# Performance work log

Hardware: AMD Instinct MI355X
Metric: run time of the kernel (lower is better)

## Reference

```python
import jax, jax.numpy as jnp
import numpy as np

B, S, H, STEPS = 4096, 169, 64, 24  # batch, input seq (window 168 + covariate row), hidden, rollout steps


def _lstm(xseq, Wih, Whh, bih, bhh, h0, c0):
    """PyTorch-style single-layer LSTM. xseq: [B,T,D] -> ([B,T,H], hT, cT). Gate order i,f,g,o."""
    xg = jnp.einsum('btd,gd->btg', xseq, Wih) + (bih + bhh)  # precompute input proj [B,T,4H]

    def step(carry, xg_t):
        h, c = carry
        g = xg_t + h @ Whh.T
        i, f, gg, o = jnp.split(g, 4, axis=-1)
        c = jax.nn.sigmoid(f) * c + jax.nn.sigmoid(i) * jnp.tanh(gg)
        h = jax.nn.sigmoid(o) * jnp.tanh(c)
        return (h, c), h

    (hT, cT), hs = jax.lax.scan(step, (h0, c0), jnp.swapaxes(xg, 0, 1))
    return jnp.swapaxes(hs, 0, 1), hT, cT


def reference(x, Wih1, Whh1, bih1, bhh1, Wih2, Whh2, bih2, bhh2, fc1_w, fc1_b, fc2_w, fc2_b):
    win, d = x[:, :-1, :], x[:, -1, :]  # [B,168,1], [B,1]
    z = jnp.zeros((x.shape[0], H), x.dtype)

    def outer(win, _):
        h1s, h1, c1 = _lstm(win, Wih1, Whh1, bih1, bhh1, z, z)
        h1s = jax.nn.relu(h1s)
        # lstm2 is seeded with lstm1's final (h, c) state, as in the torch code
        h2s, _, _ = _lstm(h1s, Wih2, Whh2, bih2, bhh2, h1, c1)
        feat = jnp.concatenate([jax.nn.relu(h2s[:, -1, :]), d], axis=1)  # [B,65]
        out = (feat @ fc1_w.T + fc1_b) @ fc2_w.T + fc2_b  # [B,1] (no relu between fc1/fc2)
        win = jnp.concatenate([win[:, 1:, :], out[:, :, None]], axis=1)  # slide window
        return win, out[:, 0]

    _, outs = jax.lax.scan(outer, win, None, length=STEPS)  # outs: [24,B]
    return jnp.swapaxes(outs, 0, 1)  # [B,24]


def setup_inputs() -> dict:
    key = jax.random.key(0)
    ks = jax.random.split(key, 14)
    bnd = 1.0 / np.sqrt(H)

    def u(k, shape):
        return jax.random.uniform(k, shape, jnp.float32, -bnd, bnd)

    return {
        'x': jax.random.normal(ks[0], (B, S, 1), jnp.float32),
        'Wih1': u(ks[1], (4 * H, 1)),
        'Whh1': u(ks[2], (4 * H, H)),
        'bih1': u(ks[3], (4 * H,)),
        'bhh1': u(ks[4], (4 * H,)),
        'Wih2': u(ks[5], (4 * H, H)),
        'Whh2': u(ks[6], (4 * H, H)),
        'bih2': u(ks[7], (4 * H,)),
        'bhh2': u(ks[8], (4 * H,)),
        'fc1_w': u(ks[9], (64, 65)),
        'fc1_b': u(ks[10], (64,)),
        'fc2_w': u(ks[11], (1, 64)),
        'fc2_b': u(ks[12], (1,)),
    }
```

## Files before the change

### kernel.cpp

```cpp
#include <hip/hip_runtime.h>
#include <stdint.h>

#define NB 16
#define WIN 168
#define NSTEPS 24
#define NBLK (4096/NB)
#define NT 512

typedef __attribute__((ext_vector_type(8))) short bf16x8;
typedef __attribute__((ext_vector_type(4))) float f32x4;

#if __has_builtin(__builtin_amdgcn_rcpf)
#define RCPF(x) __builtin_amdgcn_rcpf(x)
#else
#define RCPF(x) (1.0f / (x))
#endif
#if __has_builtin(__builtin_amdgcn_exp2f)
#define EXP2F(x) __builtin_amdgcn_exp2f(x)
#else
#define EXP2F(x) __expf((x) * 0.6931471805599453f)
#endif

__device__ __forceinline__ float sigm(float x){
  return RCPF(1.0f + EXP2F(x * -1.4426950408889634f));
}
__device__ __forceinline__ float sigtanh(float a, float b){
  float A = EXP2F(a * -1.4426950408889634f);
  float B = EXP2F(fabsf(b) * -2.8853900817779268f);
  float t = (1.0f - B) * RCPF((1.0f + A) * (1.0f + B));
  return __builtin_copysignf(t, b);
}

__device__ __forceinline__ uint32_t bf_rn(float f){
  uint32_t u = __builtin_bit_cast(uint32_t, f);
  return (u + 0x7FFFu + ((u >> 16) & 1u)) >> 16;
}
__device__ __forceinline__ float bf_f(uint32_t s){
  return __builtin_bit_cast(float, s << 16);
}
__device__ __forceinline__ void split_t(float f, uint32_t& hi, uint32_t& lo){
  uint32_t u = __builtin_bit_cast(uint32_t, f);
  hi = u >> 16;
  lo = bf_rn(f - bf_f(hi));
}
__device__ __forceinline__ void split_s(float f, short& hi, short& lo){
  uint32_t h = bf_rn(f);
  hi = (short)h;
  lo = (short)bf_rn(f - bf_f(h));
}
__device__ __forceinline__ uint32_t cvtpk2(float a, float b){
  uint32_t r;
  asm("v_cvt_pk_bf16_f32 %0, %1, %2" : "=v"(r) : "v"(a), "v"(b));
  return r;
}
__device__ __forceinline__ float hi_even(uint32_t p){
  return __builtin_bit_cast(float, p << 16);
}
__device__ __forceinline__ float hi_odd(uint32_t p){
  return __builtin_bit_cast(float, p & 0xFFFF0000u);
}
__device__ __forceinline__ f32x4 mfma16(bf16x8 a, bf16x8 b, f32x4 c){
  return __builtin_amdgcn_mfma_f32_16x16x32_bf16(a, b, c, 0, 0, 0);
}

__device__ __forceinline__ void lstm_epi(const f32x4 acc[4], float c[4], float hn[4]){
  #pragma unroll
  for (int r = 0; r < 4; r++){
    float cn = __builtin_fmaf(sigm(acc[1][r]), c[r], sigtanh(acc[0][r], acc[2][r]));
    c[r] = cn;
    hn[r] = sigtanh(acc[3][r], cn);
  }
}

#define FROW 136
#define FBLK 544
#define FB(buf,hl,kt) ((((buf)*2 + (hl))*2 + (kt)) * FBLK)
#define BUF_INTS (2*FBLK)

__global__ __launch_bounds__(NT, 2) void lstm_fused_kernel(
  const float* __restrict__ x,    const float* __restrict__ Wih1, const float* __restrict__ Whh1,
  const float* __restrict__ bih1, const float* __restrict__ bhh1,
  const float* __restrict__ Wih2, const float* __restrict__ Whh2,
  const float* __restrict__ bih2, const float* __restrict__ bhh2,
  const float* __restrict__ fc1w, const float* __restrict__ fc1b,
  const float* __restrict__ fc2w, const float* __restrict__ fc2b,
  float* __restrict__ out, short* __restrict__ hist)
{
  __shared__ __align__(16) short aS[2*2*2*FBLK];
  __shared__ __align__(16) short bS[2*2*2*FBLK];
  __shared__ float cS[64][16];
  __shared__ float win_s[WIN][NB];
  __shared__ float Hlast[NB][68];
  __shared__ float fc1w_s[64*68];
  __shared__ float dval_s[NB];

  const int tid = threadIdx.x;
  const int wv8 = tid >> 6;
  const int wv  = wv8 & 3;
  const bool isA = (wv8 < 4);
  const int ln  = tid & 63;
  const int q   = ln >> 4;
  const int n   = ln & 15;
  const int bg0 = blockIdx.x * NB;
  const int u0  = 16*wv + 4*q;
  const int kt_  = u0 >> 5;
  const int q2_  = (u0 >> 3) & 3;
  const int jj0_ = u0 & 7;
  const int rdo  = q*FROW + n*8;
  const int wro  = q2_*FROW + n*8 + jj0_;
  const int gwo  = kt_*512 + q2_*128 + n*8 + jj0_;
  const int ro   = q*128 + n*8;
  short* __restrict__ hblk = hist + (size_t)blockIdx.x * WIN * 2048;

  for (int i = tid; i < WIN*NB; i += NT){ int t = i >> 4, b = i & 15; win_s[t][b] = x[(bg0 + b)*169 + t]; }
  for (int i = tid; i < 64*65; i += NT){ int j = i / 65, k = i % 65; fc1w_s[j*68 + k] = fc1w[i]; }
  if (tid < NB) dval_s[tid] = x[(bg0 + tid)*169 + 168];

  const float fc1b_r = fc1b[ln];
  const float fc2w_r = fc2w[ln];
  const float fc2b_r = fc2b[0];

  auto fc_head = [&](int s){
    float o2[2];
    #pragma unroll
    for (int bi = 0; bi < 2; bi++){
      const int b = 2*wv8 + bi;
      float a1 = fc1b_r;
      #pragma unroll
      for (int k4 = 0; k4 < 16; k4++){
        const float* wp = &fc1w_s[ln*68 + k4*4];
        const float* hp = &Hlast[b][k4*4];
        a1 += wp[0]*hp[0] + wp[1]*hp[1] + wp[2]*hp[2] + wp[3]*hp[3];
      }
      a1 += dval_s[b] * fc1w_s[ln*68 + 64];
      float v = a1 * fc2w_r;
      #pragma unroll
      for (int off = 32; off > 0; off >>= 1) v += __shfl_xor(v, off);
      o2[bi] = v + fc2b_r;
    }
    if (ln == 0){
      #pragma unroll
      for (int bi = 0; bi < 2; bi++){
        const int b = 2*wv8 + bi;
        out[(bg0 + b)*24 + s] = o2[bi];
        win_s[s % WIN][b] = o2[bi];
      }
    }
  };

  if (isA){
    bf16x8 A1hi[4][2], A1lo[4][2], Ain1[4];
    f32x4 b1c[4];
    #pragma unroll
    for (int e = 0; e < 4; e++){
      const int ja = 64*e + 16*wv + n;
      #pragma unroll
      for (int kt = 0; kt < 2; kt++){
        const float* pw = Whh1 + ja*64 + kt*32 + q*8;
        #pragma unroll
        for (int jj = 0; jj < 8; jj++){ short h,l; split_s(pw[jj], h, l); A1hi[e][kt][jj] = h; A1lo[e][kt][jj] = l; }
      }
      bf16x8 ain = {0,0,0,0,0,0,0,0};
      if (q == 0){ short wh, wl; split_s(Wih1[ja], wh, wl); ain[0] = wh; ain[1] = wh; ain[2] = wl; }
      Ain1[e] = ain;
      const int jc = 64*e + u0;
      #pragma unroll
      for (int r = 0; r < 4; r++) b1c[e][r] = bih1[jc+r] + bhh1[jc+r];
    }
    float c1[4];

    auto lstm1 = [&](int rb, int wb, int slot, int t, bool first){
      f32x4 acc[4];
      bf16x8 bin = {0,0,0,0,0,0,0,0};
      { float xv = win_s[slot][n];
        uint32_t xp = cvtpk2(xv, xv);
        float rx = xv - hi_even(xp);
        uint32_t xq = cvtpk2(rx, rx);
        if (q == 0){ bin[0] = (short)xp; bin[1] = (short)xq; bin[2] = (short)xp; } }
      if (first){
        #pragma unroll
        for (int e = 0; e < 4; e++) acc[e] = mfma16(Ain1[e], bin, b1c[e]);
      } else {
        bf16x8 Bh0 = *(const bf16x8*)&aS[FB(rb,0,0)+rdo];
        bf16x8 Bl0 = *(const bf16x8*)&aS[FB(rb,1,0)+rdo];
        bf16x8 Bh1 = *(const bf16x8*)&aS[FB(rb,0,1)+rdo];
        bf16x8 Bl1 = *(const bf16x8*)&aS[FB(rb,1,1)+rdo];
        #pragma unroll
        for (int e = 0; e < 4; e++){
          f32x4 a = b1c[e];
          a = mfma16(A1hi[e][0], Bh0, a);
          a = mfma16(A1hi[e][0], Bl0, a);
          a = mfma16(A1lo[e][0], Bh0, a);
          a = mfma16(A1hi[e][1], Bh1, a);
          a = mfma16(A1hi[e][1], Bl1, a);
          a = mfma16(A1lo[e][1], Bh1, a);
          a = mfma16(Ain1[e], bin, a);
          acc[e] = a;
        }
      }
      float hn[4];
      lstm_epi(acc, c1, hn);
      uint32_t p01 = cvtpk2(hn[0], hn[1]);
      uint32_t p23 = cvtpk2(hn[2], hn[3]);
      float r0 = hn[0] - hi_even(p01), r1 = hn[1] - hi_odd(p01);
      float r2 = hn[2] - hi_even(p23), r3 = hn[3] - hi_odd(p23);
      uint32_t q01 = cvtpk2(r0, r1);
      uint32_t q23 = cvtpk2(r2, r3);
      *(uint2*)&aS[FB(wb,0,kt_)+wro] = make_uint2(p01, p23);
      *(uint2*)&aS[FB(wb,1,kt_)+wro] = make_uint2(q01, q23);
      uint32_t m01 = (hn[0] > 0.0f ? 0x0000FFFFu : 0u) | (hn[1] > 0.0f ? 0xFFFF0000u : 0u);
      uint32_t m23 = (hn[2] > 0.0f ? 0x0000FFFFu : 0u) | (hn[3] > 0.0f ? 0xFFFF0000u : 0u);
      short* Hp = hblk + (size_t)t * 2048;
      *(uint2*)&Hp[gwo]        = make_uint2(p01 & m01, p23 & m23);
      *(uint2*)&Hp[1024 + gwo] = make_uint2(q01 & m01, q23 & m23);
    };

    #pragma unroll
    for (int r = 0; r < 4; r++) c1[r] = 0.0f;
    __syncthreads();
    lstm1(0, 1, 0, 0, true);
    for (int t = 1; t < WIN-1; t += 2){
      __syncthreads();
      lstm1(1, 0, t, t, false);
      __syncthreads();
      lstm1(0, 1, t+1, t+1, false);
    }
    __syncthreads();
    lstm1(1, 0, WIN-1, WIN-1, false);
    #pragma unroll
    for (int r = 0; r < 4; r++) cS[u0 + r][n] = c1[r];

    for (int sg = 1; sg < NSTEPS; sg++){
      #pragma unroll
      for (int r = 0; r < 4; r++) c1[r] = 0.0f;
      int slot = sg;
      __syncthreads();
      lstm1(0, 1, slot, 0, true);
      slot++;
      for (int t = 1; t < WIN-1; t += 2){
        __syncthreads();
        lstm1(1, 0, slot, t, false);
        slot++; if (slot == WIN) slot = 0;
        __syncthreads();
        lstm1(0, 1, slot, t+1, false);
        slot++; if (slot == WIN) slot = 0;
      }
      __syncthreads();
      __syncthreads();
      fc_head(sg - 1);
      __syncthreads();
      lstm1(1, 0, slot, WIN-1, false);
      #pragma unroll
      for (int r = 0; r < 4; r++) cS[u0 + r][n] = c1[r];
    }

    for (int i = 0; i < WIN + 1; i++) __syncthreads();
    fc_head(NSTEPS - 1);

  } else {
    bf16x8 A2hi[4][4], A2lo[4][4];
    f32x4 b2c[4];
    #pragma unroll
    for (int e = 0; e < 4; e++){
      const int ja = 64*e + 16*wv + n;
      #pragma unroll
      for (int kt = 0; kt < 4; kt++){
        const float* pw = (kt < 2 ? (Wih2 + ja*64 + kt*32) : (Whh2 + ja*64 + (kt-2)*32)) + q*8;
        #pragma unroll
        for (int jj = 0; jj < 8; jj++){ short h,l; split_s(pw[jj], h, l); A2hi[e][kt][jj] = h; A2lo[e][kt][jj] = l; }
      }
      const int jc = 64*e + u0;
      #pragma unroll
      for (int r = 0; r < 4; r++) b2c[e][r] = bih2[jc+r] + bhh2[jc+r];
    }
    float c2[4];
    bf16x8 ch0, cl0, ch1, cl1, nh0, nl0, nh1, nl1;

    auto loadc = [&](int t){
      const short* Hp = hblk + (size_t)t * 2048;
      ch0 = *(const bf16x8*)&Hp[ro];
      cl0 = *(const bf16x8*)&Hp[1024 + ro];
      ch1 = *(const bf16x8*)&Hp[512 + ro];
      cl1 = *(const bf16x8*)&Hp[1536 + ro];
    };
    auto loadn = [&](int t){
      const short* Hp = hblk + (size_t)t * 2048;
      nh0 = *(const bf16x8*)&Hp[ro];
      nl0 = *(const bf16x8*)&Hp[1024 + ro];
      nh1 = *(const bf16x8*)&Hp[512 + ro];
      nl1 = *(const bf16x8*)&Hp[1536 + ro];
    };
    auto shift = [&](){ ch0 = nh0; cl0 = nl0; ch1 = nh1; cl1 = nl1; };

    auto lstm2 = [&](const short* Sr, int rb, short* Sw, int wb, bool last){
      bf16x8 L2h0 = *(const bf16x8*)&Sr[FB(rb,0,0)+rdo];
      bf16x8 L2l0 = *(const bf16x8*)&Sr[FB(rb,1,0)+rdo];
      bf16x8 L2h1 = *(const bf16x8*)&Sr[FB(rb,0,1)+rdo];
      bf16x8 L2l1 = *(const bf16x8*)&Sr[FB(rb,1,1)+rdo];
      f32x4 acc[4];
      #pragma unroll
      for (int e = 0; e < 4; e++){
        f32x4 a = b2c[e];
        a = mfma16(A2hi[e][0], ch0, a);
        a = mfma16(A2hi[e][0], cl0, a);
        a = mfma16(A2lo[e][0], ch0, a);
        a = mfma16(A2hi[e][1], ch1, a);
        a = mfma16(A2hi[e][1], cl1, a);
        a = mfma16(A2lo[e][1], ch1, a);
        a = mfma16(A2hi[e][2], L2h0, a);
        a = mfma16(A2hi[e][2], L2l0, a);
        a = mfma16(A2lo[e][2], L2h0, a);
        a = mfma16(A2hi[e][3], L2h1, a);
        a = mfma16(A2hi[e][3], L2l1, a);
        a = mfma16(A2lo[e][3], L2h1, a);
        acc[e] = a;
      }
      float hn[4];
      lstm_epi(acc, c2, hn);
      if (!last){
        uint32_t p01 = cvtpk2(hn[0], hn[1]);
        uint32_t p23 = cvtpk2(hn[2], hn[3]);
        float r0 = hn[0] - hi_even(p01), r1 = hn[1] - hi_odd(p01);
        float r2 = hn[2] - hi_even(p23), r3 = hn[3] - hi_odd(p23);
        *(uint2*)&Sw[FB(wb,0,kt_)+wro] = make_uint2(p01, p23);
        *(uint2*)&Sw[FB(wb,1,kt_)+wro] = make_uint2(cvtpk2(r0, r1), cvtpk2(r2, r3));
      } else {
        #pragma unroll
        for (int r = 0; r < 4; r++) Hlast[n][u0 + r] = fmaxf(hn[r], 0.0f);
      }
    };

    for (int i = 0; i < WIN; i++) __syncthreads();

    for (int sg = 1; sg < NSTEPS; sg++){
      loadc(0);
      loadn(1);
      __syncthreads();
      #pragma unroll
      for (int r = 0; r < 4; r++) c2[r] = cS[u0 + r][n];
      lstm2(aS, 0, bS, 1, false);
      shift();
      for (int t = 1; t < WIN-1; t += 2){
        __syncthreads();
        loadn(t + 1);
        lstm2(bS, 1, bS, 0, false);
        shift();
        __syncthreads();
        loadn(t + 2);
        lstm2(bS, 0, bS, 1, false);
        shift();
      }
      __syncthreads();
      lstm2(bS, 1, bS, 0, true);
      __syncthreads();
      fc_head(sg - 1);
      __syncthreads();
    }

    {
      loadc(0);
      loadn(1);
      __syncthreads();
      #pragma unroll
      for (int r = 0; r < 4; r++) c2[r] = cS[u0 + r][n];
      lstm2(aS, 0, bS, 1, false);
      shift();
      for (int t = 1; t < WIN-1; t += 2){
        __syncthreads();
        loadn(t + 1);
        lstm2(bS, 1, bS, 0, false);
        shift();
        __syncthreads();
        loadn(t + 2);
        lstm2(bS, 0, bS, 1, false);
        shift();
      }
      __syncthreads();
      lstm2(bS, 1, bS, 0, true);
      __syncthreads();
      fc_head(NSTEPS - 1);
    }
  }
}

__global__ __launch_bounds__(256, 1) void lstm_fallback_kernel(
  const float* __restrict__ x,    const float* __restrict__ Wih1, const float* __restrict__ Whh1,
  const float* __restrict__ bih1, const float* __restrict__ bhh1,
  const float* __restrict__ Wih2, const float* __restrict__ Whh2,
  const float* __restrict__ bih2, const float* __restrict__ bhh2,
  const float* __restrict__ fc1w, const float* __restrict__ fc1b,
  const float* __restrict__ fc2w, const float* __restrict__ fc2b,
  float* __restrict__ out)
{
  __shared__ __align__(16) short aS[2*2*2*FBLK];
  __shared__ __align__(16) short r1f[2*2*2*FBLK];
  __shared__ __align__(16) short rlf[2*2*2*FBLK];
  __shared__ float win_s[WIN][NB];
  __shared__ float Hlast[NB][68];
  __shared__ float fc1w_s[64*68];
  __shared__ float dval_s[NB];

  const int tid = threadIdx.x;
  const int wv  = tid >> 6;
  const int ln  = tid & 63;
  const int q   = ln >> 4;
  const int n   = ln & 15;
  const int bg0 = blockIdx.x * NB;
  const int u0  = 16*wv + 4*q;
  const int kt_  = u0 >> 5;
  const int q2_  = (u0 >> 3) & 3;
  const int jj0_ = u0 & 7;
  const int rdo  = q*FROW + n*8;
  const int wro  = q2_*FROW + n*8 + jj0_;

  for (int i = tid; i < WIN*NB; i += 256){ int t = i >> 4, b = i & 15; win_s[t][b] = x[(bg0 + b)*169 + t]; }
  for (int i = tid; i < 64*65; i += 256){ int j = i / 65, k = i % 65; fc1w_s[j*68 + k] = fc1w[i]; }
  if (tid < NB) dval_s[tid] = x[(bg0 + tid)*169 + 168];

  const float fc1b_r = fc1b[ln];
  const float fc2w_r = fc2w[ln];
  const float fc2b_r = fc2b[0];

  bf16x8 A1hi[4][2], A1lo[4][2], Ain1[4];
  bf16x8 A2hi[4][4], A2lo[4][4];
  f32x4 b1c[4], b2c[4];
  #pragma unroll
  for (int e = 0; e < 4; e++){
    const int ja = 64*e + 16*wv + n;
    #pragma unroll
    for (int kt = 0; kt < 2; kt++){
      const float* pw = Whh1 + ja*64 + kt*32 + q*8;
      #pragma unroll
      for (int jj = 0; jj < 8; jj++){ short h,l; split_s(pw[jj], h, l); A1hi[e][kt][jj] = h; A1lo[e][kt][jj] = l; }
    }
    #pragma unroll
    for (int kt = 0; kt < 4; kt++){
      const float* pw = (kt < 2 ? (Wih2 + ja*64 + kt*32) : (Whh2 + ja*64 + (kt-2)*32)) + q*8;
      #pragma unroll
      for (int jj = 0; jj < 8; jj++){ short h,l; split_s(pw[jj], h, l); A2hi[e][kt][jj] = h; A2lo[e][kt][jj] = l; }
    }
    bf16x8 ain = {0,0,0,0,0,0,0,0};
    if (q == 0){ short wh, wl; split_s(Wih1[ja], wh, wl); ain[0] = wh; ain[1] = wh; ain[2] = wl; }
    Ain1[e] = ain;
    const int jc = 64*e + u0;
    #pragma unroll
    for (int r = 0; r < 4; r++){
      b1c[e][r] = bih1[jc+r] + bhh1[jc+r];
      b2c[e][r] = bih2[jc+r] + bhh2[jc+r];
    }
  }

  float c1[4], c2[4], c1r[4];

  auto lstm1_step = [&](short* S, float* cst, int rb, int wb, int slot, bool relu_out){
    bf16x8 Bh0 = *(const bf16x8*)&S[FB(rb,0,0)+rdo];
    bf16x8 Bl0 = *(const bf16x8*)&S[FB(rb,1,0)+rdo];
    bf16x8 Bh1 = *(const bf16x8*)&S[FB(rb,0,1)+rdo];
    bf16x8 Bl1 = *(const bf16x8*)&S[FB(rb,1,1)+rdo];
    bf16x8 bin = {0,0,0,0,0,0,0,0};
    { float xv = win_s[slot][n]; uint32_t xh, xl; split_t(xv, xh, xl);
      if (q == 0){ bin[0] = (short)xh; bin[1] = (short)xl; bin[2] = (short)xh; } }
    f32x4 acc[4];
    #pragma unroll
    for (int e = 0; e < 4; e++){
      f32x4 a = b1c[e];
      a = mfma16(A1hi[e][0], Bh0, a);
      a = mfma16(A1hi[e][0], Bl0, a);
      a = mfma16(A1lo[e][0], Bh0, a);
      a = mfma16(A1hi[e][1], Bh1, a);
      a = mfma16(A1hi[e][1], Bl1, a);
      a = mfma16(A1lo[e][1], Bh1, a);
      a = mfma16(Ain1[e], bin, a);
      acc[e] = a;
    }
    float hn[4];
    lstm_epi(acc, cst, hn);
    uint32_t ph[4], pl[4];
    #pragma unroll
    for (int r = 0; r < 4; r++) split_t(hn[r], ph[r], pl[r]);
    *(uint2*)&S[FB(wb,0,kt_)+wro] = make_uint2(ph[0] | (ph[1]<<16), ph[2] | (ph[3]<<16));
    *(uint2*)&S[FB(wb,1,kt_)+wro] = make_uint2(pl[0] | (pl[1]<<16), pl[2] | (pl[3]<<16));
    if (relu_out){
      uint32_t sh[4], sl[4];
      #pragma unroll
      for (int r = 0; r < 4; r++){ bool pos = hn[r] > 0.0f; sh[r] = pos ? ph[r] : 0u; sl[r] = pos ? pl[r] : 0u; }
      *(uint2*)&rlf[FB(rb,0,kt_)+wro] = make_uint2(sh[0] | (sh[1]<<16), sh[2] | (sh[3]<<16));
      *(uint2*)&rlf[FB(rb,1,kt_)+wro] = make_uint2(sl[0] | (sl[1]<<16), sl[2] | (sl[3]<<16));
    }
  };

  auto lstm2_core = [&](bf16x8 L1h0, bf16x8 L1l0, bf16x8 L1h1, bf16x8 L1l1,
                        int rbuf, int wbuf, bool last){
    bf16x8 L2h0 = *(const bf16x8*)&aS[FB(rbuf,0,0)+rdo];
    bf16x8 L2l0 = *(const bf16x8*)&aS[FB(rbuf,1,0)+rdo];
    bf16x8 L2h1 = *(const bf16x8*)&aS[FB(rbuf,0,1)+rdo];
    bf16x8 L2l1 = *(const bf16x8*)&aS[FB(rbuf,1,1)+rdo];
    f32x4 acc[4];
    #pragma unroll
    for (int e = 0; e < 4; e++){
      f32x4 a = b2c[e];
      a = mfma16(A2hi[e][0], L1h0, a);
      a = mfma16(A2hi[e][0], L1l0, a);
      a = mfma16(A2lo[e][0], L1h0, a);
      a = mfma16(A2hi[e][1], L1h1, a);
      a = mfma16(A2hi[e][1], L1l1, a);
      a = mfma16(A2lo[e][1], L1h1, a);
      a = mfma16(A2hi[e][2], L2h0, a);
      a = mfma16(A2hi[e][2], L2l0, a);
      a = mfma16(A2lo[e][2], L2h0, a);
      a = mfma16(A2hi[e][3], L2h1, a);
      a = mfma16(A2hi[e][3], L2l1, a);
      a = mfma16(A2lo[e][3], L2h1, a);
      acc[e] = a;
    }
    float hn[4];
    lstm_epi(acc, c2, hn);
    if (!last){
      uint32_t ph[4], pl[4];
      #pragma unroll
      for (int r = 0; r < 4; r++) split_t(hn[r], ph[r], pl[r]);
      *(uint2*)&aS[FB(wbuf,0,kt_)+wro] = make_uint2(ph[0] | (ph[1]<<16), ph[2] | (ph[3]<<16));
      *(uint2*)&aS[FB(wbuf,1,kt_)+wro] = make_uint2(pl[0] | (pl[1]<<16), pl[2] | (pl[3]<<16));
    } else {
      #pragma unroll
      for (int r = 0; r < 4; r++) Hlast[n][u0 + r] = fmaxf(hn[r], 0.0f);
    }
  };

  for (int s = 0; s < NSTEPS; s++){
    { int* p = (int*)&aS[0];
      for (int i = tid; i < BUF_INTS; i += 256) p[i] = 0; }
    #pragma unroll
    for (int r = 0; r < 4; r++) c1[r] = 0.0f;
    int slot = s;
    for (int t = 0; t < WIN; t++){
      __syncthreads();
      lstm1_step(aS, c1, t & 1, (t & 1) ^ 1, slot, false);
      slot++; if (slot == WIN) slot = 0;
    }
    #pragma unroll
    for (int r = 0; r < 4; r++){ c2[r] = c1[r]; c1r[r] = 0.0f; }
    { int* p = (int*)&r1f[0];
      for (int i = tid; i < BUF_INTS; i += 256) p[i] = 0; }
    slot = s;
    __syncthreads();
    lstm1_step(r1f, c1r, 0, 1, slot, true);
    slot++;
    for (int i = 1; i < WIN; i++){
      __syncthreads();
      const int rb = i & 1, wb = rb ^ 1;
      lstm1_step(r1f, c1r, rb, wb, slot, true);
      bf16x8 L1h0 = *(const bf16x8*)&rlf[FB(wb,0,0)+rdo];
      bf16x8 L1l0 = *(const bf16x8*)&rlf[FB(wb,1,0)+rdo];
      bf16x8 L1h1 = *(const bf16x8*)&rlf[FB(wb,0,1)+rdo];
      bf16x8 L1l1 = *(const bf16x8*)&rlf[FB(wb,1,1)+rdo];
      lstm2_core(L1h0, L1l0, L1h1, L1l1, wb, rb, false);
      slot++; if (slot == WIN) slot = 0;
    }
    __syncthreads();
    {
      const int rb = (WIN - 1) & 1;
      bf16x8 L1h0 = *(const bf16x8*)&rlf[FB(rb,0,0)+rdo];
      bf16x8 L1l0 = *(const bf16x8*)&rlf[FB(rb,1,0)+rdo];
      bf16x8 L1h1 = *(const bf16x8*)&rlf[FB(rb,0,1)+rdo];
      bf16x8 L1l1 = *(const bf16x8*)&rlf[FB(rb,1,1)+rdo];
      lstm2_core(L1h0, L1l0, L1h1, L1l1, rb, 0, true);
    }
    __syncthreads();
    {
      float o4[4];
      #pragma unroll
      for (int bi = 0; bi < 4; bi++){
        const int b = 4*wv + bi;
        float a1 = fc1b_r;
        #pragma unroll
        for (int k4 = 0; k4 < 16; k4++){
          const float* wp = &fc1w_s[ln*68 + k4*4];
          const float* hp = &Hlast[b][k4*4];
          a1 += wp[0]*hp[0] + wp[1]*hp[1] + wp[2]*hp[2] + wp[3]*hp[3];
        }
        a1 += dval_s[b] * fc1w_s[ln*68 + 64];
        float v = a1 * fc2w_r;
        #pragma unroll
        for (int off = 32; off > 0; off >>= 1) v += __shfl_xor(v, off);
        o4[bi] = v + fc2b_r;
      }
      if (ln == 0){
        #pragma unroll
        for (int bi = 0; bi < 4; bi++){
          const int b = 4*wv + bi;
          out[(bg0 + b)*24 + s] = o4[bi];
          win_s[s % WIN][b] = o4[bi];
        }
      }
    }
  }
}

extern "C" void kernel_launch(void* const* d_in, const int* in_sizes, int n_in,
                              void* d_out, int out_size, void* d_ws, size_t ws_size,
                              hipStream_t stream) {
  (void)in_sizes; (void)n_in; (void)out_size;
  const size_t need = (size_t)NBLK * WIN * 2048 * sizeof(short);
  if (ws_size >= need){
    lstm_fused_kernel<<<dim3(NBLK), dim3(NT), 0, stream>>>(
        (const float*)d_in[0], (const float*)d_in[1], (const float*)d_in[2],
        (const float*)d_in[3], (const float*)d_in[4], (const float*)d_in[5],
        (const float*)d_in[6], (const float*)d_in[7], (const float*)d_in[8],
        (const float*)d_in[9], (const float*)d_in[10], (const float*)d_in[11],
        (const float*)d_in[12], (float*)d_out, (short*)d_ws);
  } else {
    lstm_fallback_kernel<<<dim3(NBLK), dim3(256), 0, stream>>>(
        (const float*)d_in[0], (const float*)d_in[1], (const float*)d_in[2],
        (const float*)d_in[3], (const float*)d_in[4], (const float*)d_in[5],
        (const float*)d_in[6], (const float*)d_in[7], (const float*)d_in[8],
        (const float*)d_in[9], (const float*)d_in[10], (const float*)d_in[11],
        (const float*)d_in[12], (float*)d_out);
  }
}
```

Baseline: 4.778 ms.

## Merge LSTM1/LSTM2 warp specialization into all-warps interleaved gate layout

Replaces the producer/consumer split, where 4 warps ran LSTM1 and 4 warps ran LSTM2 for the next step, with all 8 warps running both layers. Each warp now owns 8 hidden units with all four gates of a unit kept in one MFMA accumulator, so the epilogue needs no cross-lane gate exchange. The cell-state handoff through shared memory is replaced by a register copy. The intent is to halve the per-warp MFMA chain length per layer step and balance load, at the cost of more weight registers per thread and each warp doing both layers' work serially.

Measured after the change: 5.010 ms. 4.9% more time.

```diff
diff --git a/kernel.cpp b/kernel.cpp
--- a/kernel.cpp
+++ b/kernel.cpp
@@ -61,15 +61,6 @@
 }
 __device__ __forceinline__ f32x4 mfma16(bf16x8 a, bf16x8 b, f32x4 c){
   return __builtin_amdgcn_mfma_f32_16x16x32_bf16(a, b, c, 0, 0, 0);
-}
-
-__device__ __forceinline__ void lstm_epi(const f32x4 acc[4], float c[4], float hn[4]){
-  #pragma unroll
-  for (int r = 0; r < 4; r++){
-    float cn = __builtin_fmaf(sigm(acc[1][r]), c[r], sigtanh(acc[0][r], acc[2][r]));
-    c[r] = cn;
-    hn[r] = sigtanh(acc[3][r], cn);
-  }
 }
 
 #define FROW 136
@@ -88,28 +79,22 @@
 {
   __shared__ __align__(16) short aS[2*2*2*FBLK];
   __shared__ __align__(16) short bS[2*2*2*FBLK];
-  __shared__ float cS[64][16];
   __shared__ float win_s[WIN][NB];
   __shared__ float Hlast[NB][68];
   __shared__ float fc1w_s[64*68];
   __shared__ float dval_s[NB];
 
   const int tid = threadIdx.x;
-  const int wv8 = tid >> 6;
-  const int wv  = wv8 & 3;
-  const bool isA = (wv8 < 4);
+  const int w   = tid >> 6;
   const int ln  = tid & 63;
   const int q   = ln >> 4;
   const int n   = ln & 15;
   const int bg0 = blockIdx.x * NB;
-  const int u0  = 16*wv + 4*q;
-  const int kt_  = u0 >> 5;
-  const int q2_  = (u0 >> 3) & 3;
-  const int jj0_ = u0 & 7;
-  const int rdo  = q*FROW + n*8;
-  const int wro  = q2_*FROW + n*8 + jj0_;
-  const int gwo  = kt_*512 + q2_*128 + n*8 + jj0_;
-  const int ro   = q*128 + n*8;
+  const int rdo = q*FROW + n*8;
+  const int ro  = q*128 + n*8;
+  const int ktw = w >> 2;
+  const int wrw = (w&3)*FROW + n*8 + 2*q;
+  const int hwo = ktw*512 + (w&3)*128 + n*8 + 2*q;
   short* __restrict__ hblk = hist + (size_t)blockIdx.x * WIN * 2048;
 
   for (int i = tid; i < WIN*NB; i += NT){ int t = i >> 4, b = i & 15; win_s[t][b] = x[(bg0 + b)*169 + t]; }
@@ -124,7 +109,7 @@
     float o2[2];
     #pragma unroll
     for (int bi = 0; bi < 2; bi++){
-      const int b = 2*wv8 + bi;
+      const int b = 2*w + bi;
       float a1 = fc1b_r;
       #pragma unroll
       for (int k4 = 0; k4 < 16; k4++){
@@ -141,245 +126,208 @@
     if (ln == 0){
       #pragma unroll
       for (int bi = 0; bi < 2; bi++){
-        const int b = 2*wv8 + bi;
+        const int b = 2*w + bi;
         out[(bg0 + b)*24 + s] = o2[bi];
         win_s[s % WIN][b] = o2[bi];
       }
     }
   };
 
-  if (isA){
-    bf16x8 A1hi[4][2], A1lo[4][2], Ain1[4];
-    f32x4 b1c[4];
-    #pragma unroll
-    for (int e = 0; e < 4; e++){
-      const int ja = 64*e + 16*wv + n;
-      #pragma unroll
-      for (int kt = 0; kt < 2; kt++){
-        const float* pw = Whh1 + ja*64 + kt*32 + q*8;
-        #pragma unroll
-        for (int jj = 0; jj < 8; jj++){ short h,l; split_s(pw[jj], h, l); A1hi[e][kt][jj] = h; A1lo[e][kt][jj] = l; }
+  bf16x8 A1hi[2][2], A1lo[2][2], Ain1[2];
+  bf16x8 A2hi[2][4], A2lo[2][4];
+  f32x4 b1c[2], b2c[2];
+  #pragma unroll
+  for (int tu = 0; tu < 2; tu++){
+    const int jA = 64*(n&3) + 8*w + 2*(n>>2) + tu;
+    #pragma unroll
+    for (int kt = 0; kt < 2; kt++){
+      const float* pw = Whh1 + jA*64 + kt*32 + q*8;
+      #pragma unroll
+      for (int jj = 0; jj < 8; jj++){ short h,l; split_s(pw[jj], h, l); A1hi[tu][kt][jj] = h; A1lo[tu][kt][jj] = l; }
+    }
+    bf16x8 ain = {0,0,0,0,0,0,0,0};
+    if (q == 0){ short wh, wl; split_s(Wih1[jA], wh, wl); ain[0] = wh; ain[1] = wh; ain[2] = wl; }
+    Ain1[tu] = ain;
+    #pragma unroll
+    for (int kt = 0; kt < 4; kt++){
+      const float* pw = (kt < 2 ? (Wih2 + jA*64 + kt*32) : (Whh2 + jA*64 + (kt-2)*32)) + q*8;
+      #pragma unroll
+      for (int jj = 0; jj < 8; jj++){ short h,l; split_s(pw[jj], h, l); A2hi[tu][kt][jj] = h; A2lo[tu][kt][jj] = l; }
+    }
+    const int U = 8*w + 2*q + tu;
+    #pragma unroll
+    for (int r = 0; r < 4; r++){
+      b1c[tu][r] = bih1[64*r + U] + bhh1[64*r + U];
+      b2c[tu][r] = bih2[64*r + U] + bhh2[64*r + U];
+    }
+  }
+
+  float c1[2], c1sav[2], c2[2];
+  bf16x8 hA0, lA0, hA1, lA1, hB0, lB0, hB1, lB1;
+
+  auto loadA = [&](int t){
+    const short* Hp = hblk + (size_t)t * 2048;
+    hA0 = *(const bf16x8*)&Hp[ro];
+    lA0 = *(const bf16x8*)&Hp[1024 + ro];
+    hA1 = *(const bf16x8*)&Hp[512 + ro];
+    lA1 = *(const bf16x8*)&Hp[1536 + ro];
+  };
+  auto loadB = [&](int t){
+    const short* Hp = hblk + (size_t)t * 2048;
+    hB0 = *(const bf16x8*)&Hp[ro];
+    lB0 = *(const bf16x8*)&Hp[1024 + ro];
+    hB1 = *(const bf16x8*)&Hp[512 + ro];
+    lB1 = *(const bf16x8*)&Hp[1536 + ro];
+  };
+
+  auto lstm1 = [&](int rb, int wb, int slot, int t, bool first){
+    bf16x8 bin = {0,0,0,0,0,0,0,0};
+    { float xv = win_s[slot][n];
+      uint32_t xp = cvtpk2(xv, xv);
+      float rx = xv - hi_even(xp);
+      uint32_t xq = cvtpk2(rx, rx);
+      if (q == 0){ bin[0] = (short)xp; bin[1] = (short)xq; bin[2] = (short)xp; } }
+    f32x4 acc[2];
+    if (first){
+      #pragma unroll
+      for (int tu = 0; tu < 2; tu++) acc[tu] = mfma16(Ain1[tu], bin, b1c[tu]);
+    } else {
+      bf16x8 Bh0 = *(const bf16x8*)&aS[FB(rb,0,0)+rdo];
+      bf16x8 Bl0 = *(const bf16x8*)&aS[FB(rb,1,0)+rdo];
+      bf16x8 Bh1 = *(const bf16x8*)&aS[FB(rb,0,1)+rdo];
+      bf16x8 Bl1 = *(const bf16x8*)&aS[FB(rb,1,1)+rdo];
+      #pragma unroll
+      for (int tu = 0; tu < 2; tu++){
+        f32x4 a = b1c[tu];
+        a = mfma16(A1hi[tu][0], Bh0, a);
+        a = mfma16(A1hi[tu][0], Bl0, a);
+        a = mfma16(A1lo[tu][0], Bh0, a);
+        a = mfma16(A1hi[tu][1], Bh1, a);
+        a = mfma16(A1hi[tu][1], Bl1, a);
+        a = mfma16(A1lo[tu][1], Bh1, a);
+        a = mfma16(Ain1[tu], bin, a);
+        acc[tu] = a;
       }
-      bf16x8 ain = {0,0,0,0,0,0,0,0};
-      if (q == 0){ short wh, wl; split_s(Wih1[ja], wh, wl); ain[0] = wh; ain[1] = wh; ain[2] = wl; }
-      Ain1[e] = ain;
-      const int jc = 64*e + u0;
-      #pragma unroll
-      for (int r = 0; r < 4; r++) b1c[e][r] = bih1[jc+r] + bhh1[jc+r];
-    }
-    float c1[4];
-
-    auto lstm1 = [&](int rb, int wb, int slot, int t, bool first){
-      f32x4 acc[4];
-      bf16x8 bin = {0,0,0,0,0,0,0,0};
-      { float xv = win_s[slot][n];
-        uint32_t xp = cvtpk2(xv, xv);
-        float rx = xv - hi_even(xp);
-        uint32_t xq = cvtpk2(rx, rx);
-        if (q == 0){ bin[0] = (short)xp; bin[1] = (short)xq; bin[2] = (short)xp; } }
-      if (first){
-        #pragma unroll
-        for (int e = 0; e < 4; e++) acc[e] = mfma16(Ain1[e], bin, b1c[e]);
-      } else {
-        bf16x8 Bh0 = *(const bf16x8*)&aS[FB(rb,0,0)+rdo];
-        bf16x8 Bl0 = *(const bf16x8*)&aS[FB(rb,1,0)+rdo];
-        bf16x8 Bh1 = *(const bf16x8*)&aS[FB(rb,0,1)+rdo];
-        bf16x8 Bl1 = *(const bf16x8*)&aS[FB(rb,1,1)+rdo];
-        #pragma unroll
-        for (int e = 0; e < 4; e++){
-          f32x4 a = b1c[e];
-          a = mfma16(A1hi[e][0], Bh0, a);
-          a = mfma16(A1hi[e][0], Bl0, a);
-          a = mfma16(A1lo[e][0], Bh0, a);
-          a = mfma16(A1hi[e][1], Bh1, a);
-          a = mfma16(A1hi[e][1], Bl1, a);
-          a = mfma16(A1lo[e][1], Bh1, a);
-          a = mfma16(Ain1[e], bin, a);
-          acc[e] = a;
-        }
-      }
-      float hn[4];
-      lstm_epi(acc, c1, hn);
-      uint32_t p01 = cvtpk2(hn[0], hn[1]);
-      uint32_t p23 = cvtpk2(hn[2], hn[3]);
-      float r0 = hn[0] - hi_even(p01), r1 = hn[1] - hi_odd(p01);
-      float r2 = hn[2] - hi_even(p23), r3 = hn[3] - hi_odd(p23);
-      uint32_t q01 = cvtpk2(r0, r1);
-      uint32_t q23 = cvtpk2(r2, r3);
-      *(uint2*)&aS[FB(wb,0,kt_)+wro] = make_uint2(p01, p23);
-      *(uint2*)&aS[FB(wb,1,kt_)+wro] = make_uint2(q01, q23);
-      uint32_t m01 = (hn[0] > 0.0f ? 0x0000FFFFu : 0u) | (hn[1] > 0.0f ? 0xFFFF0000u : 0u);
-      uint32_t m23 = (hn[2] > 0.0f ? 0x0000FFFFu : 0u) | (hn[3] > 0.0f ? 0xFFFF0000u : 0u);
-      short* Hp = hblk + (size_t)t * 2048;
-      *(uint2*)&Hp[gwo]        = make_uint2(p01 & m01, p23 & m23);
-      *(uint2*)&Hp[1024 + gwo] = make_uint2(q01 & m01, q23 & m23);
-    };
-
-    #pragma unroll
-    for (int r = 0; r < 4; r++) c1[r] = 0.0f;
-    __syncthreads();
-    lstm1(0, 1, 0, 0, true);
+    }
+    float hn[2];
+    #pragma unroll
+    for (int tu = 0; tu < 2; tu++){
+      float cn = __builtin_fmaf(sigm(acc[tu][1]), c1[tu], sigtanh(acc[tu][0], acc[tu][2]));
+      c1[tu] = cn;
+      hn[tu] = sigtanh(acc[tu][3], cn);
+    }
+    uint32_t p  = cvtpk2(hn[0], hn[1]);
+    float r0 = hn[0] - hi_even(p), r1 = hn[1] - hi_odd(p);
+    uint32_t ql = cvtpk2(r0, r1);
+    *(uint32_t*)&aS[FB(wb,0,ktw)+wrw] = p;
+    *(uint32_t*)&aS[FB(wb,1,ktw)+wrw] = ql;
+    uint32_t m = (hn[0] > 0.0f ? 0x0000FFFFu : 0u) | (hn[1] > 0.0f ? 0xFFFF0000u : 0u);
+    short* Hp = hblk + (size_t)t * 2048;
+    *(uint32_t*)&Hp[hwo]        = p  & m;
+    *(uint32_t*)&Hp[1024 + hwo] = ql & m;
+  };
+
+  auto lstm2 = [&](bf16x8 h0, bf16x8 l0, bf16x8 h1, bf16x8 l1,
+                   const short* Sr, int rb, short* Sw, int wb, bool last){
+    bf16x8 Sh0 = *(const bf16x8*)&Sr[FB(rb,0,0)+rdo];
+    bf16x8 Sl0 = *(const bf16x8*)&Sr[FB(rb,1,0)+rdo];
+    bf16x8 Sh1 = *(const bf16x8*)&Sr[FB(rb,0,1)+rdo];
+    bf16x8 Sl1 = *(const bf16x8*)&Sr[FB(rb,1,1)+rdo];
+    f32x4 acc[2];
+    #pragma unroll
+    for (int tu = 0; tu < 2; tu++){
+      f32x4 a = b2c[tu];
+      a = mfma16(A2hi[tu][0], h0, a);
+      a = mfma16(A2hi[tu][0], l0, a);
+      a = mfma16(A2lo[tu][0], h0, a);
+      a = mfma16(A2hi[tu][1], h1, a);
+      a = mfma16(A2hi[tu][1], l1, a);
+      a = mfma16(A2lo[tu][1], h1, a);
+      a = mfma16(A2hi[tu][2], Sh0, a);
+      a = mfma16(A2hi[tu][2], Sl0, a);
+      a = mfma16(A2lo[tu][2], Sh0, a);
+      a = mfma16(A2hi[tu][3], Sh1, a);
+      a = mfma16(A2hi[tu][3], Sl1, a);
+      a = mfma16(A2lo[tu][3], Sh1, a);
+      acc[tu] = a;
+    }
+    float hn[2];
+    #pragma unroll
+    for (int tu = 0; tu < 2; tu++){
+      float cn = __builtin_fmaf(sigm(acc[tu][1]), c2[tu], sigtanh(acc[tu][0], acc[tu][2]));
+      c2[tu] = cn;
+      hn[tu] = sigtanh(acc[tu][3], cn);
+    }
+    if (!last){
+      uint32_t p  = cvtpk2(hn[0], hn[1]);
+      float r0 = hn[0] - hi_even(p), r1 = hn[1] - hi_odd(p);
+      uint32_t ql = cvtpk2(r0, r1);
+      *(uint32_t*)&Sw[FB(wb,0,ktw)+wrw] = p;
+      *(uint32_t*)&Sw[FB(wb,1,ktw)+wrw] = ql;
+    } else {
+      const int U0 = 8*w + 2*q;
+      Hlast[n][U0]     = fmaxf(hn[0], 0.0f);
+      Hlast[n][U0 + 1] = fmaxf(hn[1], 0.0f);
+    }
+  };
+
+  c1[0] = 0.0f; c1[1] = 0.0f;
+  __syncthreads();
+  lstm1(0, 1, 0, 0, true);
+  for (int t = 1; t < WIN-1; t += 2){
+    __syncthreads();
+    lstm1(1, 0, t, t, false);
+    __syncthreads();
+    lstm1(0, 1, t+1, t+1, false);
+  }
+  __syncthreads();
+  lstm1(1, 0, WIN-1, WIN-1, false);
+  c1sav[0] = c1[0]; c1sav[1] = c1[1];
+
+  for (int sg = 1; sg < NSTEPS; sg++){
+    c2[0] = c1sav[0]; c2[1] = c1sav[1];
+    c1[0] = 0.0f;     c1[1] = 0.0f;
+    loadA(0); loadB(1);
+    int slot = sg;
+    __syncthreads();
+    lstm1(0, 1, slot, 0, true); slot++;
+    lstm2(hA0, lA0, hA1, lA1, aS, 0, bS, 1, false);
     for (int t = 1; t < WIN-1; t += 2){
       __syncthreads();
-      lstm1(1, 0, t, t, false);
+      loadA(t + 1);
+      lstm1(1, 0, slot, t, false); slot++; if (slot == WIN) slot = 0;
+      lstm2(hB0, lB0, hB1, lB1, bS, 1, bS, 0, false);
       __syncthreads();
-      lstm1(0, 1, t+1, t+1, false);
-    }
-    __syncthreads();
-    lstm1(1, 0, WIN-1, WIN-1, false);
-    #pragma unroll
-    for (int r = 0; r < 4; r++) cS[u0 + r][n] = c1[r];
-
-    for (int sg = 1; sg < NSTEPS; sg++){
-      #pragma unroll
-      for (int r = 0; r < 4; r++) c1[r] = 0.0f;
-      int slot = sg;
+      loadB(t + 2);
+      lstm1(0, 1, slot, t+1, false); slot++; if (slot == WIN) slot = 0;
+      lstm2(hA0, lA0, hA1, lA1, bS, 0, bS, 1, false);
+    }
+    __syncthreads();
+    lstm2(hB0, lB0, hB1, lB1, bS, 1, bS, 0, true);
+    __syncthreads();
+    fc_head(sg - 1);
+    __syncthreads();
+    lstm1(1, 0, slot, WIN-1, false);
+    c1sav[0] = c1[0]; c1sav[1] = c1[1];
+  }
+
+  {
+    c2[0] = c1sav[0]; c2[1] = c1sav[1];
+    loadA(0); loadB(1);
+    __syncthreads();
+    lstm2(hA0, lA0, hA1, lA1, aS, 0, bS, 1, false);
+    for (int t = 1; t < WIN-1; t += 2){
       __syncthreads();
-      lstm1(0, 1, slot, 0, true);
-      slot++;
-      for (int t = 1; t < WIN-1; t += 2){
-        __syncthreads();
-        lstm1(1, 0, slot, t, false);
-        slot++; if (slot == WIN) slot = 0;
-        __syncthreads();
-        lstm1(0, 1, slot, t+1, false);
-        slot++; if (slot == WIN) slot = 0;
-      }
+      loadA(t + 1);
+      lstm2(hB0, lB0, hB1, lB1, bS, 1, bS, 0, false);
       __syncthreads();
-      __syncthreads();
-      fc_head(sg - 1);
-      __syncthreads();
-      lstm1(1, 0, slot, WIN-1, false);
-      #pragma unroll
-      for (int r = 0; r < 4; r++) cS[u0 + r][n] = c1[r];
-    }
-
-    for (int i = 0; i < WIN + 1; i++) __syncthreads();
+      loadB(t + 2);
+      lstm2(hA0, lA0, hA1, lA1, bS, 0, bS, 1, false);
+    }
+    __syncthreads();
+    lstm2(hB0, lB0, hB1, lB1, bS, 1, bS, 0, true);
+    __syncthreads();
     fc_head(NSTEPS - 1);
-
-  } else {
-    bf16x8 A2hi[4][4], A2lo[4][4];
-    f32x4 b2c[4];
-    #pragma unroll
-    for (int e = 0; e < 4; e++){
-      const int ja = 64*e + 16*wv + n;
-      #pragma unroll
-      for (int kt = 0; kt < 4; kt++){
-        const float* pw = (kt < 2 ? (Wih2 + ja*64 + kt*32) : (Whh2 + ja*64 + (kt-2)*32)) + q*8;
-        #pragma unroll
-        for (int jj = 0; jj < 8; jj++){ short h,l; split_s(pw[jj], h, l); A2hi[e][kt][jj] = h; A2lo[e][kt][jj] = l; }
-      }
-      const int jc = 64*e + u0;
-      #pragma unroll
-      for (int r = 0; r < 4; r++) b2c[e][r] = bih2[jc+r] + bhh2[jc+r];
-    }
-    float c2[4];
-    bf16x8 ch0, cl0, ch1, cl1, nh0, nl0, nh1, nl1;
-
-    auto loadc = [&](int t){
-      const short* Hp = hblk + (size_t)t * 2048;
-      ch0 = *(const bf16x8*)&Hp[ro];
-      cl0 = *(const bf16x8*)&Hp[1024 + ro];
-      ch1 = *(const bf16x8*)&Hp[512 + ro];
-      cl1 = *(const bf16x8*)&Hp[1536 + ro];
-    };
-    auto loadn = [&](int t){
-      const short* Hp = hblk + (size_t)t * 2048;
-      nh0 = *(const bf16x8*)&Hp[ro];
-      nl0 = *(const bf16x8*)&Hp[1024 + ro];
-      nh1 = *(const bf16x8*)&Hp[512 + ro];
-      nl1 = *(const bf16x8*)&Hp[1536 + ro];
-    };
-    auto shift = [&](){ ch0 = nh0; cl0 = nl0; ch1 = nh1; cl1 = nl1; };
-
-    auto lstm2 = [&](const short* Sr, int rb, short* Sw, int wb, bool last){
-      bf16x8 L2h0 = *(const bf16x8*)&Sr[FB(rb,0,0)+rdo];
-      bf16x8 L2l0 = *(const bf16x8*)&Sr[FB(rb,1,0)+rdo];
-      bf16x8 L2h1 = *(const bf16x8*)&Sr[FB(rb,0,1)+rdo];
-      bf16x8 L2l1 = *(const bf16x8*)&Sr[FB(rb,1,1)+rdo];
-      f32x4 acc[4];
-      #pragma unroll
-      for (int e = 0; e < 4; e++){
-        f32x4 a = b2c[e];
-        a = mfma16(A2hi[e][0], ch0, a);
-        a = mfma16(A2hi[e][0], cl0, a);
-        a = mfma16(A2lo[e][0], ch0, a);
-        a = mfma16(A2hi[e][1], ch1, a);
-        a = mfma16(A2hi[e][1], cl1, a);
-        a = mfma16(A2lo[e][1], ch1, a);
-        a = mfma16(A2hi[e][2], L2h0, a);
-        a = mfma16(A2hi[e][2], L2l0, a);
-        a = mfma16(A2lo[e][2], L2h0, a);
-        a = mfma16(A2hi[e][3], L2h1, a);
-        a = mfma16(A2hi[e][3], L2l1, a);
-        a = mfma16(A2lo[e][3], L2h1, a);
-        acc[e] = a;
-      }
-      float hn[4];
-      lstm_epi(acc, c2, hn);
-      if (!last){
-        uint32_t p01 = cvtpk2(hn[0], hn[1]);
-        uint32_t p23 = cvtpk2(hn[2], hn[3]);
-        float r0 = hn[0] - hi_even(p01), r1 = hn[1] - hi_odd(p01);
-        float r2 = hn[2] - hi_even(p23), r3 = hn[3] - hi_odd(p23);
-        *(uint2*)&Sw[FB(wb,0,kt_)+wro] = make_uint2(p01, p23);
-        *(uint2*)&Sw[FB(wb,1,kt_)+wro] = make_uint2(cvtpk2(r0, r1), cvtpk2(r2, r3));
-      } else {
-        #pragma unroll
-        for (int r = 0; r < 4; r++) Hlast[n][u0 + r] = fmaxf(hn[r], 0.0f);
-      }
-    };
-
-    for (int i = 0; i < WIN; i++) __syncthreads();
-
-    for (int sg = 1; sg < NSTEPS; sg++){
-      loadc(0);
-      loadn(1);
-      __syncthreads();
-      #pragma unroll
-      for (int r = 0; r < 4; r++) c2[r] = cS[u0 + r][n];
-      lstm2(aS, 0, bS, 1, false);
-      shift();
-      for (int t = 1; t < WIN-1; t += 2){
-        __syncthreads();
-        loadn(t + 1);
-        lstm2(bS, 1, bS, 0, false);
-        shift();
-        __syncthreads();
-        loadn(t + 2);
-        lstm2(bS, 0, bS, 1, false);
-        shift();
-      }
-      __syncthreads();
-      lstm2(bS, 1, bS, 0, true);
-      __syncthreads();
-      fc_head(sg - 1);
-      __syncthreads();
-    }
-
-    {
-      loadc(0);
-      loadn(1);
-      __syncthreads();
-      #pragma unroll
-      for (int r = 0; r < 4; r++) c2[r] = cS[u0 + r][n];
-      lstm2(aS, 0, bS, 1, false);
-      shift();
-      for (int t = 1; t < WIN-1; t += 2){
-        __syncthreads();
-        loadn(t + 1);
-        lstm2(bS, 1, bS, 0, false);
-        shift();
-        __syncthreads();
-        loadn(t + 2);
-        lstm2(bS, 0, bS, 1, false);
-        shift();
-      }
-      __syncthreads();
-      lstm2(bS, 1, bS, 0, true);
-      __syncthreads();
-      fc_head(NSTEPS - 1);
-    }
   }
 }
 
@@ -474,7 +422,12 @@
       acc[e] = a;
     }
     float hn[4];
-    lstm_epi(acc, cst, hn);
+    #pragma unroll
+    for (int r = 0; r < 4; r++){
+      float cn = __builtin_fmaf(sigm(acc[1][r]), cst[r], sigtanh(acc[0][r], acc[2][r]));
+      cst[r] = cn;
+      hn[r] = sigtanh(acc[3][r], cn);
+    }
     uint32_t ph[4], pl[4];
     #pragma unroll
     for (int r = 0; r < 4; r++) split_t(hn[r], ph[r], pl[r]);
@@ -514,7 +467,12 @@
       acc[e] = a;
     }
     float hn[4];
-    lstm_epi(acc, c2, hn);
+    #pragma unroll
+    for (int r = 0; r < 4; r++){
+      float cn = __builtin_fmaf(sigm(acc[1][r]), c2[r], sigtanh(acc[0][r], acc[2][r]));
+      c2[r] = cn;
+      hn[r] = sigtanh(acc[3][r], cn);
+    }
     if (!last){
       uint32_t ph[4], pl[4];
       #pragma unroll
```
